# Performance work log

Hardware: AMD Instinct MI355X
Metric: run time of the kernel (lower is better)

The kernel has to match this reference:

```python
import jax, jax.numpy as jnp
import numpy as np

# Module config (matches init_kwargs)
B, CIN, COUT = 16, 32, 32
H, W = 128, 128
M1, M2 = 64, 64          # modes
KH, KW = 3, 3            # bandwidth
TRIL = 1
P1 = M1 + KH - 1 - 2 * TRIL   # pad_slices extent per dim = 64
P2 = M2 + KW - 1 - 2 * TRIL


def setup_inputs() -> dict:
    key = jax.random.key(0)
    k = jax.random.split(key, 6)
    scale = 1.0 / (CIN * COUT)
    return {
        "u": jax.random.normal(k[0], (B, CIN, H, W), dtype=jnp.float32),
        "A1": jax.random.normal(k[1], (H, H), dtype=jnp.float32) / np.sqrt(H).astype(np.float32),
        "A2": jax.random.normal(k[2], (W, W), dtype=jnp.float32) / np.sqrt(W).astype(np.float32),
        "B1": jax.random.normal(k[3], (H, M1), dtype=jnp.float32) / np.sqrt(M1).astype(np.float32),
        "B2": jax.random.normal(k[4], (W, M2), dtype=jnp.float32) / np.sqrt(M2).astype(np.float32),
        "weights": scale * jax.random.uniform(k[5], (CIN * KH * KW, COUT, M1 * M2), dtype=jnp.float32),
    }


def _unfold(x):
    """torch.nn.Unfold(kernel_size=(KH,KW), padding=TRIL) on [B,C,P1,P2].
    Returns [B, C*KH*KW, M1*M2] with channel-major (c, i, j) ordering."""
    xp = jnp.pad(x, ((0, 0), (0, 0), (TRIL, TRIL), (TRIL, TRIL)))
    # stack KH*KW shifted views -> [B, C, KH*KW, M1, M2]
    patches = jnp.stack(
        [xp[:, :, i:i + M1, j:j + M2] for i in range(KH) for j in range(KW)],
        axis=2,
    )
    return patches.reshape(x.shape[0], x.shape[1] * KH * KW, M1 * M2)


def reference(u, A1, A2, B1, B2, weights):
    # Forward transform T(u, X_dims): separable linear transform over last 2 dims
    b = jnp.einsum('bchw,mh,kw->bcmk', u, A1, A2)          # [B, CIN, H, W] spectral coeffs
    # pad_slices: first (modes + bandwidth - 1 - 2*triL) frequencies per dim
    bp = b[:, :, :P1, :P2]
    # quasi_diag_mul: unfold (im2col) + per-mode banded matmul
    xpad = _unfold(bp)                                      # [B, CIN*KH*KW, M1*M2]
    out = jnp.einsum('bix,iox->box', xpad, weights)         # [B, COUT, M1*M2]
    out = out.reshape(B, COUT, M1, M2)                      # scatter into zeros fills all modes
    # Inverse transform T.inv(out, X_dims)
    return jnp.einsum('bcmk,hm,wk->bchw', out, B1, B2)      # [B, COUT, H, W]
```

## Files before the change

### kernel.cpp

```cpp
#include <hip/hip_runtime.h>
#include <cstddef>


#define NB 16
#define NCIN 32
#define NCOUT 32

__device__ __forceinline__ float dpp_shr1(float x) {
  int r = __builtin_amdgcn_update_dpp(0, __float_as_int(x), 0x111, 0xF, 0xF, true);
  return __int_as_float(r);
}
__device__ __forceinline__ float dpp_shl1(float x) {
  int r = __builtin_amdgcn_update_dpp(0, __float_as_int(x), 0x101, 0xF, 0xF, true);
  return __int_as_float(r);
}

__global__ __launch_bounds__(256) void k1_spectral(const float* __restrict__ u,
                                                   const float* __restrict__ A1,
                                                   const float* __restrict__ A2,
                                                   float* __restrict__ bpi) {
  __shared__ float a2t[128 * 68];
  __shared__ float t_s[128 * 68];
  const int tid = threadIdx.x;
  const int bc = blockIdx.x;
  const float* up = u + (size_t)bc * 16384;

#pragma unroll
  for (int it = 0; it < 8; ++it) {
    int f = it * 256 + tid;
    int k = f >> 5;
    int w4 = (f & 31) * 4;
    float4 v = *(const float4*)(A2 + k * 128 + w4);
    a2t[(w4 + 0) * 68 + k] = v.x;
    a2t[(w4 + 1) * 68 + k] = v.y;
    a2t[(w4 + 2) * 68 + k] = v.z;
    a2t[(w4 + 3) * 68 + k] = v.w;
  }
  __syncthreads();

  {
    const int h0 = (tid >> 4) * 8;
    const int k0 = (tid & 15) * 4;
    float acc[8][4] = {};
#pragma unroll 2
    for (int w4 = 0; w4 < 128; w4 += 4) {
      float4 uv[8];
#pragma unroll
      for (int i = 0; i < 8; ++i)
        uv[i] = *(const float4*)(up + (h0 + i) * 128 + w4);
      float4 av[4];
#pragma unroll
      for (int dw = 0; dw < 4; ++dw)
        av[dw] = *(const float4*)(a2t + (w4 + dw) * 68 + k0);
#pragma unroll
      for (int i = 0; i < 8; ++i) {
        const float* up_ = (const float*)&uv[i];
#pragma unroll
        for (int dw = 0; dw < 4; ++dw) {
          const float* ap = (const float*)&av[dw];
          float uval = up_[dw];
#pragma unroll
          for (int j = 0; j < 4; ++j) acc[i][j] += uval * ap[j];
        }
      }
    }
#pragma unroll
    for (int i = 0; i < 8; ++i)
      *(float4*)(t_s + (h0 + i) * 68 + k0) =
          make_float4(acc[i][0], acc[i][1], acc[i][2], acc[i][3]);
  }
  __syncthreads();

  {
    const int m0 = (tid >> 4) * 4;
    const int k0 = (tid & 15) * 4;
    float acc[4][4] = {};
#pragma unroll 2
    for (int h4 = 0; h4 < 128; h4 += 4) {
      float4 a1v[4];
#pragma unroll
      for (int i = 0; i < 4; ++i)
        a1v[i] = *(const float4*)(A1 + (m0 + i) * 128 + h4);
      float4 tv[4];
#pragma unroll
      for (int dh = 0; dh < 4; ++dh)
        tv[dh] = *(const float4*)(t_s + (h4 + dh) * 68 + k0);
#pragma unroll
      for (int i = 0; i < 4; ++i) {
        const float* ap = (const float*)&a1v[i];
#pragma unroll
        for (int dh = 0; dh < 4; ++dh) {
          const float* tp = (const float*)&tv[dh];
          float aval = ap[dh];
#pragma unroll
          for (int j = 0; j < 4; ++j) acc[i][j] += aval * tp[j];
        }
      }
    }
    float* bp = bpi + (size_t)bc * 4096;
#pragma unroll
    for (int i = 0; i < 4; ++i)
      *(float4*)(bp + (m0 + i) * 64 + k0) =
          make_float4(acc[i][0], acc[i][1], acc[i][2], acc[i][3]);
  }
}

__global__ __launch_bounds__(256) void k2_conv(const float* __restrict__ bpi,
                                               const float* __restrict__ Wt,
                                               float* __restrict__ out2) {
  const int tid = threadIdx.x;
  const int lane = tid & 63;
  const int wv = tid >> 6;
  const int xjg = lane & 15;
  const int lbg = lane >> 4;
  const int bid = blockIdx.x;
  const int xi = ((bid & 7) << 3) | (bid >> 3);
  const int og = blockIdx.y;
  const int bg = wv >> 1;
  const int op = wv & 1;
  const int o0 = og * 4 + op * 2;
  const int b0 = bg * 8 + lbg * 2;

  float acc[2][2][4] = {};

  for (int c = 0; c < NCIN; ++c) {
    float4 xv[2][3];
#pragma unroll
    for (int ki = 0; ki < 3; ++ki) {
      const int row = xi - 1 + ki;
      const bool valid = (row >= 0) && (row < 64);
#pragma unroll
      for (int rb = 0; rb < 2; ++rb) {
        if (valid)
          xv[rb][ki] = *(const float4*)(bpi +
              (((size_t)(b0 + rb) * NCIN + c) * 64 + row) * 64 + xjg * 4);
        else
          xv[rb][ki] = make_float4(0.f, 0.f, 0.f, 0.f);
      }
    }
    float4 wr[9][2];
    const float* wbase = Wt + (((size_t)c * 9) * NCOUT + o0) * 4096 + xi * 64 + xjg * 4;
#pragma unroll
    for (int t = 0; t < 9; ++t) {
#pragma unroll
      for (int oo = 0; oo < 2; ++oo)
        wr[t][oo] = *(const float4*)(wbase + ((size_t)t * NCOUT + oo) * 4096);
    }
#pragma unroll
    for (int ki = 0; ki < 3; ++ki) {
#pragma unroll
      for (int rb = 0; rb < 2; ++rb) {
        float xw[6];
        xw[1] = xv[rb][ki].x; xw[2] = xv[rb][ki].y;
        xw[3] = xv[rb][ki].z; xw[4] = xv[rb][ki].w;
        xw[0] = dpp_shr1(xv[rb][ki].w);
        xw[5] = dpp_shl1(xv[rb][ki].x);
#pragma unroll
        for (int kj = 0; kj < 3; ++kj) {
          const int t = ki * 3 + kj;
#pragma unroll
          for (int oo = 0; oo < 2; ++oo) {
            const float* w = (const float*)&wr[t][oo];
#pragma unroll
            for (int x = 0; x < 4; ++x)
              acc[rb][oo][x] += xw[x + kj] * w[x];
          }
        }
      }
    }
  }
#pragma unroll
  for (int rb = 0; rb < 2; ++rb)
#pragma unroll
    for (int oo = 0; oo < 2; ++oo)
      *(float4*)(out2 + ((size_t)(b0 + rb) * NCOUT + (o0 + oo)) * 4096 + xi * 64 + xjg * 4) =
          make_float4(acc[rb][oo][0], acc[rb][oo][1], acc[rb][oo][2], acc[rb][oo][3]);
}

__global__ __launch_bounds__(256) void k3_recon(const float* __restrict__ out2,
                                                const float* __restrict__ B1,
                                                const float* __restrict__ B2,
                                                float* __restrict__ outp) {
  __shared__ float b2t[64 * 132];
  __shared__ float t2[64 * 132];
  const int tid = threadIdx.x;
  const int bc = blockIdx.x;

#pragma unroll
  for (int it = 0; it < 8; ++it) {
    int f = it * 256 + tid;
    int w = f >> 4;
    int k4 = (f & 15) * 4;
    float4 v = *(const float4*)(B2 + w * 64 + k4);
    b2t[(k4 + 0) * 132 + w] = v.x;
    b2t[(k4 + 1) * 132 + w] = v.y;
    b2t[(k4 + 2) * 132 + w] = v.z;
    b2t[(k4 + 3) * 132 + w] = v.w;
  }
  __syncthreads();

  {
    const int m0 = (tid >> 5) * 8;
    const int w0 = (tid & 31) * 4;
    float acc[8][4] = {};
    const float* o2 = out2 + (size_t)bc * 4096;
#pragma unroll 2
    for (int k4 = 0; k4 < 64; k4 += 4) {
      float4 a[8];
#pragma unroll
      for (int i = 0; i < 8; ++i) a[i] = *(const float4*)(o2 + (m0 + i) * 64 + k4);
      float4 bb[4];
#pragma unroll
      for (int dk = 0; dk < 4; ++dk) bb[dk] = *(const float4*)(b2t + (k4 + dk) * 132 + w0);
#pragma unroll
      for (int i = 0; i < 8; ++i) {
        const float* ap = (const float*)&a[i];
#pragma unroll
        for (int dk = 0; dk < 4; ++dk) {
          const float* bp = (const float*)&bb[dk];
          float aval = ap[dk];
#pragma unroll
          for (int j = 0; j < 4; ++j) acc[i][j] += aval * bp[j];
        }
      }
    }
    __syncthreads();
#pragma unroll
    for (int i = 0; i < 8; ++i)
      *(float4*)(t2 + (m0 + i) * 132 + w0) =
          make_float4(acc[i][0], acc[i][1], acc[i][2], acc[i][3]);
  }
  __syncthreads();

  {
    const int h0 = (tid >> 4) * 8;
    const int w0 = (tid & 15) * 8;
    float acc[8][8] = {};
#pragma unroll 2
    for (int m = 0; m < 64; m += 4) {
      float4 a[8];
#pragma unroll
      for (int i = 0; i < 8; ++i) a[i] = *(const float4*)(B1 + (h0 + i) * 64 + m);
      float4 bb[4][2];
#pragma unroll
      for (int dm = 0; dm < 4; ++dm) {
        bb[dm][0] = *(const float4*)(t2 + (m + dm) * 132 + w0);
        bb[dm][1] = *(const float4*)(t2 + (m + dm) * 132 + w0 + 4);
      }
#pragma unroll
      for (int i = 0; i < 8; ++i) {
        const float* ap = (const float*)&a[i];
#pragma unroll
        for (int dm = 0; dm < 4; ++dm) {
          const float* b0p = (const float*)&bb[dm][0];
          const float* b1p = (const float*)&bb[dm][1];
          float aval = ap[dm];
#pragma unroll
          for (int j = 0; j < 4; ++j) {
            acc[i][j]     += aval * b0p[j];
            acc[i][4 + j] += aval * b1p[j];
          }
        }
      }
    }
    float* rp = outp + (size_t)bc * 16384;
#pragma unroll
    for (int i = 0; i < 8; ++i) {
      *(float4*)(rp + (h0 + i) * 128 + w0) =
          make_float4(acc[i][0], acc[i][1], acc[i][2], acc[i][3]);
      *(float4*)(rp + (h0 + i) * 128 + w0 + 4) =
          make_float4(acc[i][4], acc[i][5], acc[i][6], acc[i][7]);
    }
  }
}

extern "C" void kernel_launch(void* const* d_in, const int* in_sizes, int n_in,
                              void* d_out, int out_size, void* d_ws, size_t ws_size,
                              hipStream_t stream) {
  (void)in_sizes; (void)n_in; (void)out_size; (void)ws_size;
  const float* u  = (const float*)d_in[0];
  const float* A1 = (const float*)d_in[1];
  const float* A2 = (const float*)d_in[2];
  const float* B1 = (const float*)d_in[3];
  const float* B2 = (const float*)d_in[4];
  const float* Wt = (const float*)d_in[5];
  float* out = (float*)d_out;

  float* bpi  = (float*)d_ws;
  float* out2 = (float*)((char*)d_ws + (size_t)NB * NCIN * 4096 * sizeof(float));

  k1_spectral<<<NB * NCIN, 256, 0, stream>>>(u, A1, A2, bpi);
  k2_conv<<<dim3(64, 8), 256, 0, stream>>>(bpi, Wt, out2);
  k3_recon<<<NB * NCOUT, 256, 0, stream>>>(out2, B1, B2, out);
}
```

Before: 359.1 us.

## Split conv input channels across grid z with partial sums reduced in recon

The conv kernel now splits the input-channel loop across blockIdx.z, growing the grid from 512 to up to 2048 blocks. Each split writes its own partial-output slab, and the reconstruction kernel sums the partial slabs as it loads them. Stores of intermediates switch to nontemporal writes. This trades extra workspace and extra partial-sum traffic for more parallelism in the conv stage, which previously launched few blocks for a 256-CU GPU.

```diff
diff --git a/kernel.cpp b/kernel.cpp
--- a/kernel.cpp
+++ b/kernel.cpp
@@ -6,6 +6,8 @@
 #define NCIN 32
 #define NCOUT 32
 
+typedef float f32x4 __attribute__((ext_vector_type(4)));
+
 __device__ __forceinline__ float dpp_shr1(float x) {
   int r = __builtin_amdgcn_update_dpp(0, __float_as_int(x), 0x111, 0xF, 0xF, true);
   return __int_as_float(r);
@@ -13,6 +15,13 @@
 __device__ __forceinline__ float dpp_shl1(float x) {
   int r = __builtin_amdgcn_update_dpp(0, __float_as_int(x), 0x101, 0xF, 0xF, true);
   return __int_as_float(r);
+}
+__device__ __forceinline__ float4 f4add(float4 a, float4 b) {
+  return make_float4(a.x + b.x, a.y + b.y, a.z + b.z, a.w + b.w);
+}
+__device__ __forceinline__ void nt_store4(float* p, float a, float b, float c, float d) {
+  f32x4 v; v.x = a; v.y = b; v.z = c; v.w = d;
+  __builtin_nontemporal_store(v, (f32x4*)p);
 }
 
 __global__ __launch_bounds__(256) void k1_spectral(const float* __restrict__ u,
@@ -100,14 +109,14 @@
     float* bp = bpi + (size_t)bc * 4096;
 #pragma unroll
     for (int i = 0; i < 4; ++i)
-      *(float4*)(bp + (m0 + i) * 64 + k0) =
-          make_float4(acc[i][0], acc[i][1], acc[i][2], acc[i][3]);
-  }
-}
-
+      nt_store4(bp + (m0 + i) * 64 + k0, acc[i][0], acc[i][1], acc[i][2], acc[i][3]);
+  }
+}
+
+template <int CPC>
 __global__ __launch_bounds__(256) void k2_conv(const float* __restrict__ bpi,
                                                const float* __restrict__ Wt,
-                                               float* __restrict__ out2) {
+                                               float* __restrict__ out2p) {
   const int tid = threadIdx.x;
   const int lane = tid & 63;
   const int wv = tid >> 6;
@@ -116,6 +125,8 @@
   const int bid = blockIdx.x;
   const int xi = ((bid & 7) << 3) | (bid >> 3);
   const int og = blockIdx.y;
+  const int cz = blockIdx.z;
+  const int c0 = cz * CPC;
   const int bg = wv >> 1;
   const int op = wv & 1;
   const int o0 = og * 4 + op * 2;
@@ -123,7 +134,8 @@
 
   float acc[2][2][4] = {};
 
-  for (int c = 0; c < NCIN; ++c) {
+  for (int cc = 0; cc < CPC; ++cc) {
+    const int c = c0 + cc;
     float4 xv[2][3];
 #pragma unroll
     for (int ki = 0; ki < 3; ++ki) {
@@ -169,15 +181,17 @@
       }
     }
   }
+  float* dst0 = out2p + (size_t)cz * (NB * NCOUT * 4096);
 #pragma unroll
   for (int rb = 0; rb < 2; ++rb)
 #pragma unroll
     for (int oo = 0; oo < 2; ++oo)
-      *(float4*)(out2 + ((size_t)(b0 + rb) * NCOUT + (o0 + oo)) * 4096 + xi * 64 + xjg * 4) =
-          make_float4(acc[rb][oo][0], acc[rb][oo][1], acc[rb][oo][2], acc[rb][oo][3]);
-}
-
-__global__ __launch_bounds__(256) void k3_recon(const float* __restrict__ out2,
+      nt_store4(dst0 + ((size_t)(b0 + rb) * NCOUT + (o0 + oo)) * 4096 + xi * 64 + xjg * 4,
+                acc[rb][oo][0], acc[rb][oo][1], acc[rb][oo][2], acc[rb][oo][3]);
+}
+
+template <int NCH>
+__global__ __launch_bounds__(256) void k3_recon(const float* __restrict__ out2p,
                                                 const float* __restrict__ B1,
                                                 const float* __restrict__ B2,
                                                 float* __restrict__ outp) {
@@ -185,6 +199,7 @@
   __shared__ float t2[64 * 132];
   const int tid = threadIdx.x;
   const int bc = blockIdx.x;
+  const size_t PSTR = (size_t)NB * NCOUT * 4096;
 
 #pragma unroll
   for (int it = 0; it < 8; ++it) {
@@ -203,12 +218,17 @@
     const int m0 = (tid >> 5) * 8;
     const int w0 = (tid & 31) * 4;
     float acc[8][4] = {};
-    const float* o2 = out2 + (size_t)bc * 4096;
+    const float* o2 = out2p + (size_t)bc * 4096;
 #pragma unroll 2
     for (int k4 = 0; k4 < 64; k4 += 4) {
       float4 a[8];
 #pragma unroll
-      for (int i = 0; i < 8; ++i) a[i] = *(const float4*)(o2 + (m0 + i) * 64 + k4);
+      for (int i = 0; i < 8; ++i) {
+        a[i] = *(const float4*)(o2 + (m0 + i) * 64 + k4);
+#pragma unroll
+        for (int p = 1; p < NCH; ++p)
+          a[i] = f4add(a[i], *(const float4*)(o2 + p * PSTR + (m0 + i) * 64 + k4));
+      }
       float4 bb[4];
 #pragma unroll
       for (int dk = 0; dk < 4; ++dk) bb[dk] = *(const float4*)(b2t + (k4 + dk) * 132 + w0);
@@ -277,7 +297,7 @@
 extern "C" void kernel_launch(void* const* d_in, const int* in_sizes, int n_in,
                               void* d_out, int out_size, void* d_ws, size_t ws_size,
                               hipStream_t stream) {
-  (void)in_sizes; (void)n_in; (void)out_size; (void)ws_size;
+  (void)in_sizes; (void)n_in; (void)out_size;
   const float* u  = (const float*)d_in[0];
   const float* A1 = (const float*)d_in[1];
   const float* A2 = (const float*)d_in[2];
@@ -286,10 +306,20 @@
   const float* Wt = (const float*)d_in[5];
   float* out = (float*)d_out;
 
-  float* bpi  = (float*)d_ws;
-  float* out2 = (float*)((char*)d_ws + (size_t)NB * NCIN * 4096 * sizeof(float));
+  const size_t SEG = (size_t)NB * NCIN * 4096 * sizeof(float);
+  float* bpi   = (float*)d_ws;
+  float* out2p = (float*)((char*)d_ws + SEG);
 
   k1_spectral<<<NB * NCIN, 256, 0, stream>>>(u, A1, A2, bpi);
-  k2_conv<<<dim3(64, 8), 256, 0, stream>>>(bpi, Wt, out2);
-  k3_recon<<<NB * NCOUT, 256, 0, stream>>>(out2, B1, B2, out);
-}
+
+  if (ws_size >= SEG * 5) {
+    k2_conv<8><<<dim3(64, 8, 4), 256, 0, stream>>>(bpi, Wt, out2p);
+    k3_recon<4><<<NB * NCOUT, 256, 0, stream>>>(out2p, B1, B2, out);
+  } else if (ws_size >= SEG * 3) {
+    k2_conv<16><<<dim3(64, 8, 2), 256, 0, stream>>>(bpi, Wt, out2p);
+    k3_recon<2><<<NB * NCOUT, 256, 0, stream>>>(out2p, B1, B2, out);
+  } else {
+    k2_conv<32><<<dim3(64, 8, 1), 256, 0, stream>>>(bpi, Wt, out2p);
+    k3_recon<1><<<NB * NCOUT, 256, 0, stream>>>(out2p, B1, B2, out);
+  }
+}
```

Measured after the change: 394.3 us. +9.8%, slower.

## Double-buffer global loads in all three kernels and use nontemporal stores

Applied to the files above, without the earlier changes.

Each GEMM-like loop in k1 and k3 now prefetches the next chunk of global operands into a second register buffer while computing on the current one. k2 ping-pongs two full load buffers across input channels and raises occupancy hints via launch_bounds(256,2). Intermediate outputs of k1 and k2 use nontemporal stores. The k3 second stage remaps columns so each thread reads two float4s 64 apart, which is meant to reduce LDS bank conflicts. The extra buffers raise register pressure, which may cut occupancy or cause spills.

```diff
diff --git a/kernel.cpp b/kernel.cpp
--- a/kernel.cpp
+++ b/kernel.cpp
@@ -6,6 +6,8 @@
 #define NCIN 32
 #define NCOUT 32
 
+typedef float f32x4 __attribute__((ext_vector_type(4)));
+
 __device__ __forceinline__ float dpp_shr1(float x) {
   int r = __builtin_amdgcn_update_dpp(0, __float_as_int(x), 0x111, 0xF, 0xF, true);
   return __int_as_float(r);
@@ -13,6 +15,10 @@
 __device__ __forceinline__ float dpp_shl1(float x) {
   int r = __builtin_amdgcn_update_dpp(0, __float_as_int(x), 0x101, 0xF, 0xF, true);
   return __int_as_float(r);
+}
+__device__ __forceinline__ void nt_store4(float* p, float a, float b, float c, float d) {
+  f32x4 v; v.x = a; v.y = b; v.z = c; v.w = d;
+  __builtin_nontemporal_store(v, (f32x4*)p);
 }
 
 __global__ __launch_bounds__(256) void k1_spectral(const float* __restrict__ u,
@@ -42,25 +48,48 @@
     const int h0 = (tid >> 4) * 8;
     const int k0 = (tid & 15) * 4;
     float acc[8][4] = {};
-#pragma unroll 2
-    for (int w4 = 0; w4 < 128; w4 += 4) {
-      float4 uv[8];
-#pragma unroll
-      for (int i = 0; i < 8; ++i)
-        uv[i] = *(const float4*)(up + (h0 + i) * 128 + w4);
-      float4 av[4];
-#pragma unroll
-      for (int dw = 0; dw < 4; ++dw)
-        av[dw] = *(const float4*)(a2t + (w4 + dw) * 68 + k0);
-#pragma unroll
-      for (int i = 0; i < 8; ++i) {
-        const float* up_ = (const float*)&uv[i];
-#pragma unroll
-        for (int dw = 0; dw < 4; ++dw) {
-          const float* ap = (const float*)&av[dw];
-          float uval = up_[dw];
-#pragma unroll
-          for (int j = 0; j < 4; ++j) acc[i][j] += uval * ap[j];
+    float4 uvA[8], uvB[8];
+#pragma unroll
+    for (int i = 0; i < 8; ++i) uvA[i] = *(const float4*)(up + (h0 + i) * 128 + 0);
+
+#pragma unroll 1
+    for (int w4 = 0; w4 < 128; w4 += 8) {
+#pragma unroll
+      for (int i = 0; i < 8; ++i) uvB[i] = *(const float4*)(up + (h0 + i) * 128 + w4 + 4);
+      {
+        float4 av[4];
+#pragma unroll
+        for (int dw = 0; dw < 4; ++dw) av[dw] = *(const float4*)(a2t + (w4 + dw) * 68 + k0);
+#pragma unroll
+        for (int i = 0; i < 8; ++i) {
+          const float* up_ = (const float*)&uvA[i];
+#pragma unroll
+          for (int dw = 0; dw < 4; ++dw) {
+            const float* ap = (const float*)&av[dw];
+            float uval = up_[dw];
+#pragma unroll
+            for (int j = 0; j < 4; ++j) acc[i][j] += uval * ap[j];
+          }
+        }
+      }
+      if (w4 + 8 < 128) {
+#pragma unroll
+        for (int i = 0; i < 8; ++i) uvA[i] = *(const float4*)(up + (h0 + i) * 128 + w4 + 8);
+      }
+      {
+        float4 av[4];
+#pragma unroll
+        for (int dw = 0; dw < 4; ++dw) av[dw] = *(const float4*)(a2t + (w4 + 4 + dw) * 68 + k0);
+#pragma unroll
+        for (int i = 0; i < 8; ++i) {
+          const float* up_ = (const float*)&uvB[i];
+#pragma unroll
+          for (int dw = 0; dw < 4; ++dw) {
+            const float* ap = (const float*)&av[dw];
+            float uval = up_[dw];
+#pragma unroll
+            for (int j = 0; j < 4; ++j) acc[i][j] += uval * ap[j];
+          }
         }
       }
     }
@@ -75,39 +104,115 @@
     const int m0 = (tid >> 4) * 4;
     const int k0 = (tid & 15) * 4;
     float acc[4][4] = {};
-#pragma unroll 2
-    for (int h4 = 0; h4 < 128; h4 += 4) {
-      float4 a1v[4];
-#pragma unroll
-      for (int i = 0; i < 4; ++i)
-        a1v[i] = *(const float4*)(A1 + (m0 + i) * 128 + h4);
-      float4 tv[4];
-#pragma unroll
-      for (int dh = 0; dh < 4; ++dh)
-        tv[dh] = *(const float4*)(t_s + (h4 + dh) * 68 + k0);
-#pragma unroll
-      for (int i = 0; i < 4; ++i) {
-        const float* ap = (const float*)&a1v[i];
-#pragma unroll
-        for (int dh = 0; dh < 4; ++dh) {
-          const float* tp = (const float*)&tv[dh];
-          float aval = ap[dh];
-#pragma unroll
-          for (int j = 0; j < 4; ++j) acc[i][j] += aval * tp[j];
+    float4 aA[4], aB[4];
+#pragma unroll
+    for (int i = 0; i < 4; ++i) aA[i] = *(const float4*)(A1 + (m0 + i) * 128 + 0);
+
+#pragma unroll 1
+    for (int h4 = 0; h4 < 128; h4 += 8) {
+#pragma unroll
+      for (int i = 0; i < 4; ++i) aB[i] = *(const float4*)(A1 + (m0 + i) * 128 + h4 + 4);
+      {
+        float4 tv[4];
+#pragma unroll
+        for (int dh = 0; dh < 4; ++dh) tv[dh] = *(const float4*)(t_s + (h4 + dh) * 68 + k0);
+#pragma unroll
+        for (int i = 0; i < 4; ++i) {
+          const float* ap = (const float*)&aA[i];
+#pragma unroll
+          for (int dh = 0; dh < 4; ++dh) {
+            const float* tp = (const float*)&tv[dh];
+            float aval = ap[dh];
+#pragma unroll
+            for (int j = 0; j < 4; ++j) acc[i][j] += aval * tp[j];
+          }
+        }
+      }
+      if (h4 + 8 < 128) {
+#pragma unroll
+        for (int i = 0; i < 4; ++i) aA[i] = *(const float4*)(A1 + (m0 + i) * 128 + h4 + 8);
+      }
+      {
+        float4 tv[4];
+#pragma unroll
+        for (int dh = 0; dh < 4; ++dh) tv[dh] = *(const float4*)(t_s + (h4 + 4 + dh) * 68 + k0);
+#pragma unroll
+        for (int i = 0; i < 4; ++i) {
+          const float* ap = (const float*)&aB[i];
+#pragma unroll
+          for (int dh = 0; dh < 4; ++dh) {
+            const float* tp = (const float*)&tv[dh];
+            float aval = ap[dh];
+#pragma unroll
+            for (int j = 0; j < 4; ++j) acc[i][j] += aval * tp[j];
+          }
         }
       }
     }
     float* bp = bpi + (size_t)bc * 4096;
 #pragma unroll
     for (int i = 0; i < 4; ++i)
-      *(float4*)(bp + (m0 + i) * 64 + k0) =
-          make_float4(acc[i][0], acc[i][1], acc[i][2], acc[i][3]);
-  }
-}
-
-__global__ __launch_bounds__(256) void k2_conv(const float* __restrict__ bpi,
-                                               const float* __restrict__ Wt,
-                                               float* __restrict__ out2) {
+      nt_store4(bp + (m0 + i) * 64 + k0, acc[i][0], acc[i][1], acc[i][2], acc[i][3]);
+  }
+}
+
+struct K2Buf {
+  float4 xv[2][3];
+  float4 wr[9][2];
+};
+
+__device__ __forceinline__ void k2_load(K2Buf& B, const float* __restrict__ bpi,
+                                        const float* __restrict__ Wt,
+                                        int c, int xi, int b0, int o0, int xjg) {
+#pragma unroll
+  for (int ki = 0; ki < 3; ++ki) {
+    const int row = xi - 1 + ki;
+    const bool valid = (row >= 0) && (row < 64);
+#pragma unroll
+    for (int rb = 0; rb < 2; ++rb) {
+      if (valid)
+        B.xv[rb][ki] = *(const float4*)(bpi +
+            (((size_t)(b0 + rb) * NCIN + c) * 64 + row) * 64 + xjg * 4);
+      else
+        B.xv[rb][ki] = make_float4(0.f, 0.f, 0.f, 0.f);
+    }
+  }
+  const float* wbase = Wt + (((size_t)c * 9) * NCOUT + o0) * 4096 + xi * 64 + xjg * 4;
+#pragma unroll
+  for (int t = 0; t < 9; ++t)
+#pragma unroll
+    for (int oo = 0; oo < 2; ++oo)
+      B.wr[t][oo] = *(const float4*)(wbase + ((size_t)t * NCOUT + oo) * 4096);
+}
+
+__device__ __forceinline__ void k2_compute(const K2Buf& B, float acc[2][2][4]) {
+#pragma unroll
+  for (int ki = 0; ki < 3; ++ki) {
+#pragma unroll
+    for (int rb = 0; rb < 2; ++rb) {
+      float xw[6];
+      xw[1] = B.xv[rb][ki].x; xw[2] = B.xv[rb][ki].y;
+      xw[3] = B.xv[rb][ki].z; xw[4] = B.xv[rb][ki].w;
+      xw[0] = dpp_shr1(B.xv[rb][ki].w);
+      xw[5] = dpp_shl1(B.xv[rb][ki].x);
+#pragma unroll
+      for (int kj = 0; kj < 3; ++kj) {
+        const int t = ki * 3 + kj;
+#pragma unroll
+        for (int oo = 0; oo < 2; ++oo) {
+          const float* w = (const float*)&B.wr[t][oo];
+#pragma unroll
+          for (int x = 0; x < 4; ++x)
+            acc[rb][oo][x] += xw[x + kj] * w[x];
+        }
+      }
+    }
+  }
+}
+
+__global__ __launch_bounds__(256, 2) void k2_conv(const float* __restrict__ bpi,
+                                                  const float* __restrict__ Wt,
+                                                  float* __restrict__ out2) {
   const int tid = threadIdx.x;
   const int lane = tid & 63;
   const int wv = tid >> 6;
@@ -122,59 +227,24 @@
   const int b0 = bg * 8 + lbg * 2;
 
   float acc[2][2][4] = {};
-
-  for (int c = 0; c < NCIN; ++c) {
-    float4 xv[2][3];
-#pragma unroll
-    for (int ki = 0; ki < 3; ++ki) {
-      const int row = xi - 1 + ki;
-      const bool valid = (row >= 0) && (row < 64);
-#pragma unroll
-      for (int rb = 0; rb < 2; ++rb) {
-        if (valid)
-          xv[rb][ki] = *(const float4*)(bpi +
-              (((size_t)(b0 + rb) * NCIN + c) * 64 + row) * 64 + xjg * 4);
-        else
-          xv[rb][ki] = make_float4(0.f, 0.f, 0.f, 0.f);
-      }
-    }
-    float4 wr[9][2];
-    const float* wbase = Wt + (((size_t)c * 9) * NCOUT + o0) * 4096 + xi * 64 + xjg * 4;
-#pragma unroll
-    for (int t = 0; t < 9; ++t) {
-#pragma unroll
-      for (int oo = 0; oo < 2; ++oo)
-        wr[t][oo] = *(const float4*)(wbase + ((size_t)t * NCOUT + oo) * 4096);
-    }
-#pragma unroll
-    for (int ki = 0; ki < 3; ++ki) {
-#pragma unroll
-      for (int rb = 0; rb < 2; ++rb) {
-        float xw[6];
-        xw[1] = xv[rb][ki].x; xw[2] = xv[rb][ki].y;
-        xw[3] = xv[rb][ki].z; xw[4] = xv[rb][ki].w;
-        xw[0] = dpp_shr1(xv[rb][ki].w);
-        xw[5] = dpp_shl1(xv[rb][ki].x);
-#pragma unroll
-        for (int kj = 0; kj < 3; ++kj) {
-          const int t = ki * 3 + kj;
-#pragma unroll
-          for (int oo = 0; oo < 2; ++oo) {
-            const float* w = (const float*)&wr[t][oo];
-#pragma unroll
-            for (int x = 0; x < 4; ++x)
-              acc[rb][oo][x] += xw[x + kj] * w[x];
-          }
-        }
-      }
-    }
-  }
+  K2Buf A, Bb;
+  k2_load(A,  bpi, Wt, 0, xi, b0, o0, xjg);
+  k2_load(Bb, bpi, Wt, 1, xi, b0, o0, xjg);
+
+#pragma unroll 1
+  for (int c = 0; c < NCIN; c += 2) {
+    k2_compute(A, acc);
+    if (c + 2 < NCIN) k2_load(A, bpi, Wt, c + 2, xi, b0, o0, xjg);
+    k2_compute(Bb, acc);
+    if (c + 3 < NCIN) k2_load(Bb, bpi, Wt, c + 3, xi, b0, o0, xjg);
+  }
+
 #pragma unroll
   for (int rb = 0; rb < 2; ++rb)
 #pragma unroll
     for (int oo = 0; oo < 2; ++oo)
-      *(float4*)(out2 + ((size_t)(b0 + rb) * NCOUT + (o0 + oo)) * 4096 + xi * 64 + xjg * 4) =
-          make_float4(acc[rb][oo][0], acc[rb][oo][1], acc[rb][oo][2], acc[rb][oo][3]);
+      nt_store4(out2 + ((size_t)(b0 + rb) * NCOUT + (o0 + oo)) * 4096 + xi * 64 + xjg * 4,
+                acc[rb][oo][0], acc[rb][oo][1], acc[rb][oo][2], acc[rb][oo][3]);
 }
 
 __global__ __launch_bounds__(256) void k3_recon(const float* __restrict__ out2,
@@ -204,23 +274,48 @@
     const int w0 = (tid & 31) * 4;
     float acc[8][4] = {};
     const float* o2 = out2 + (size_t)bc * 4096;
-#pragma unroll 2
-    for (int k4 = 0; k4 < 64; k4 += 4) {
-      float4 a[8];
-#pragma unroll
-      for (int i = 0; i < 8; ++i) a[i] = *(const float4*)(o2 + (m0 + i) * 64 + k4);
-      float4 bb[4];
-#pragma unroll
-      for (int dk = 0; dk < 4; ++dk) bb[dk] = *(const float4*)(b2t + (k4 + dk) * 132 + w0);
-#pragma unroll
-      for (int i = 0; i < 8; ++i) {
-        const float* ap = (const float*)&a[i];
-#pragma unroll
-        for (int dk = 0; dk < 4; ++dk) {
-          const float* bp = (const float*)&bb[dk];
-          float aval = ap[dk];
-#pragma unroll
-          for (int j = 0; j < 4; ++j) acc[i][j] += aval * bp[j];
+    float4 aA[8], aB[8];
+#pragma unroll
+    for (int i = 0; i < 8; ++i) aA[i] = *(const float4*)(o2 + (m0 + i) * 64 + 0);
+
+#pragma unroll 1
+    for (int k4 = 0; k4 < 64; k4 += 8) {
+#pragma unroll
+      for (int i = 0; i < 8; ++i) aB[i] = *(const float4*)(o2 + (m0 + i) * 64 + k4 + 4);
+      {
+        float4 bb[4];
+#pragma unroll
+        for (int dk = 0; dk < 4; ++dk) bb[dk] = *(const float4*)(b2t + (k4 + dk) * 132 + w0);
+#pragma unroll
+        for (int i = 0; i < 8; ++i) {
+          const float* ap = (const float*)&aA[i];
+#pragma unroll
+          for (int dk = 0; dk < 4; ++dk) {
+            const float* bp = (const float*)&bb[dk];
+            float aval = ap[dk];
+#pragma unroll
+            for (int j = 0; j < 4; ++j) acc[i][j] += aval * bp[j];
+          }
+        }
+      }
+      if (k4 + 8 < 64) {
+#pragma unroll
+        for (int i = 0; i < 8; ++i) aA[i] = *(const float4*)(o2 + (m0 + i) * 64 + k4 + 8);
+      }
+      {
+        float4 bb[4];
+#pragma unroll
+        for (int dk = 0; dk < 4; ++dk) bb[dk] = *(const float4*)(b2t + (k4 + 4 + dk) * 132 + w0);
+#pragma unroll
+        for (int i = 0; i < 8; ++i) {
+          const float* ap = (const float*)&aB[i];
+#pragma unroll
+          for (int dk = 0; dk < 4; ++dk) {
+            const float* bp = (const float*)&bb[dk];
+            float aval = ap[dk];
+#pragma unroll
+            for (int j = 0; j < 4; ++j) acc[i][j] += aval * bp[j];
+          }
         }
       }
     }
@@ -234,31 +329,63 @@
 
   {
     const int h0 = (tid >> 4) * 8;
-    const int w0 = (tid & 15) * 8;
+    const int w0 = (tid & 15) * 4;
     float acc[8][8] = {};
-#pragma unroll 2
-    for (int m = 0; m < 64; m += 4) {
-      float4 a[8];
-#pragma unroll
-      for (int i = 0; i < 8; ++i) a[i] = *(const float4*)(B1 + (h0 + i) * 64 + m);
-      float4 bb[4][2];
-#pragma unroll
-      for (int dm = 0; dm < 4; ++dm) {
-        bb[dm][0] = *(const float4*)(t2 + (m + dm) * 132 + w0);
-        bb[dm][1] = *(const float4*)(t2 + (m + dm) * 132 + w0 + 4);
-      }
-#pragma unroll
-      for (int i = 0; i < 8; ++i) {
-        const float* ap = (const float*)&a[i];
+    float4 aA[8], aB[8];
+#pragma unroll
+    for (int i = 0; i < 8; ++i) aA[i] = *(const float4*)(B1 + (h0 + i) * 64 + 0);
+
+#pragma unroll 1
+    for (int m = 0; m < 64; m += 8) {
+#pragma unroll
+      for (int i = 0; i < 8; ++i) aB[i] = *(const float4*)(B1 + (h0 + i) * 64 + m + 4);
+      {
+        float4 bb0[4], bb1[4];
 #pragma unroll
         for (int dm = 0; dm < 4; ++dm) {
-          const float* b0p = (const float*)&bb[dm][0];
-          const float* b1p = (const float*)&bb[dm][1];
-          float aval = ap[dm];
-#pragma unroll
-          for (int j = 0; j < 4; ++j) {
-            acc[i][j]     += aval * b0p[j];
-            acc[i][4 + j] += aval * b1p[j];
+          bb0[dm] = *(const float4*)(t2 + (m + dm) * 132 + w0);
+          bb1[dm] = *(const float4*)(t2 + (m + dm) * 132 + w0 + 64);
+        }
+#pragma unroll
+        for (int i = 0; i < 8; ++i) {
+          const float* ap = (const float*)&aA[i];
+#pragma unroll
+          for (int dm = 0; dm < 4; ++dm) {
+            const float* b0p = (const float*)&bb0[dm];
+            const float* b1p = (const float*)&bb1[dm];
+            float aval = ap[dm];
+#pragma unroll
+            for (int j = 0; j < 4; ++j) {
+              acc[i][j]     += aval * b0p[j];
+              acc[i][4 + j] += aval * b1p[j];
+            }
+          }
+        }
+      }
+      if (m + 8 < 64) {
+#pragma unroll
+        for (int i = 0; i < 8; ++i) aA[i] = *(const float4*)(B1 + (h0 + i) * 64 + m + 8);
+      }
+      {
+        float4 bb0[4], bb1[4];
+#pragma unroll
+        for (int dm = 0; dm < 4; ++dm) {
+          bb0[dm] = *(const float4*)(t2 + (m + 4 + dm) * 132 + w0);
+          bb1[dm] = *(const float4*)(t2 + (m + 4 + dm) * 132 + w0 + 64);
+        }
+#pragma unroll
+        for (int i = 0; i < 8; ++i) {
+          const float* ap = (const float*)&aB[i];
+#pragma unroll
+          for (int dm = 0; dm < 4; ++dm) {
+            const float* b0p = (const float*)&bb0[dm];
+            const float* b1p = (const float*)&bb1[dm];
+            float aval = ap[dm];
+#pragma unroll
+            for (int j = 0; j < 4; ++j) {
+              acc[i][j]     += aval * b0p[j];
+              acc[i][4 + j] += aval * b1p[j];
+            }
           }
         }
       }
@@ -268,7 +395,7 @@
     for (int i = 0; i < 8; ++i) {
       *(float4*)(rp + (h0 + i) * 128 + w0) =
           make_float4(acc[i][0], acc[i][1], acc[i][2], acc[i][3]);
-      *(float4*)(rp + (h0 + i) * 128 + w0 + 4) =
+      *(float4*)(rp + (h0 + i) * 128 + w0 + 64) =
           make_float4(acc[i][4], acc[i][5], acc[i][6], acc[i][7]);
     }
   }
@@ -286,8 +413,9 @@
   const float* Wt = (const float*)d_in[5];
   float* out = (float*)d_out;
 
+  const size_t SEG = (size_t)NB * NCIN * 4096 * sizeof(float);
   float* bpi  = (float*)d_ws;
-  float* out2 = (float*)((char*)d_ws + (size_t)NB * NCIN * 4096 * sizeof(float));
+  float* out2 = (float*)((char*)d_ws + SEG);
 
   k1_spectral<<<NB * NCIN, 256, 0, stream>>>(u, A1, A2, bpi);
   k2_conv<<<dim3(64, 8), 256, 0, stream>>>(bpi, Wt, out2);
```

New measurement: 1.386 ms. 3.86x slower.
